# Kernel optimization log

Hardware: AMD Instinct MI355X
Metric: run time of the kernel (lower is better)

Reference implementation:

```python
import jax, jax.numpy as jnp
import numpy as np

D = 128          # hidden_dim
H = 4            # num attention heads (torch default nhead=4 in this module)
DH = D // H
NA = 4096        # author nodes
NP = 100000      # paper nodes
EAP = 500000     # author->paper edges
EPA = 500000     # paper->author edges
DFF = 2048       # TransformerEncoderLayer FFN dim (torch default)
OUT = 16
IN_A = 128
IN_P = 256
EPS = 1e-5


def layer_norm(x, g, b):
    mu = jnp.mean(x, -1, keepdims=True)
    var = jnp.mean((x - mu) ** 2, -1, keepdims=True)
    return (x - mu) / jnp.sqrt(var + EPS) * g + b


def scatter_mean(vals, idx, n):
    # torch_scatter 'mean': empty segments yield 0
    s = jax.ops.segment_sum(vals, idx, num_segments=n)
    c = jax.ops.segment_sum(jnp.ones((vals.shape[0], 1), vals.dtype), idx, num_segments=n)
    return s / jnp.maximum(c, 1.0)


def metapath_layer(x_src, x_dst, src, dst, Wv, bv, Wo, bo, g, b):
    # nn.MultiheadAttention applied per-edge with seq_len=1 (query/key/value are
    # [1, E, D]); softmax over a single key is identically 1, so the attention
    # output is exactly out_proj(v_proj(x_src[src])) -- q/k projections have no
    # effect on the output (and zero gradient).
    v = x_src[src] @ Wv.T + bv            # [E, D] gather + value projection
    attn = v @ Wo.T + bo                  # output projection
    agg = scatter_mean(attn, dst, x_dst.shape[0])
    return layer_norm(agg + x_dst, g, b)


def fusion_layer(x, Wqkv, bqkv, Wo, bo, W1, b1, W2, b2, g1, bt1, g2, bt2):
    # torch TransformerEncoderLayer defaults: post-norm, relu, batch_first=False,
    # so x: [S=NA (seq), M (batch = #metapaths), D].
    S, M, _ = x.shape
    qkv = x @ Wqkv.T + bqkv               # [S, M, 3D]
    q, k, v = jnp.split(qkv, 3, axis=-1)
    q = q.reshape(S, M, H, DH)
    k = k.reshape(S, M, H, DH)
    v = v.reshape(S, M, H, DH)
    scores = jnp.einsum('smhd,tmhd->mhst', q, k) / np.float32(np.sqrt(DH))
    a = jax.nn.softmax(scores, axis=-1)
    ctx = jnp.einsum('mhst,tmhd->smhd', a, v).reshape(S, M, D)
    x = layer_norm(x + ctx @ Wo.T + bo, g1, bt1)
    ff = jax.nn.relu(x @ W1.T + b1) @ W2.T + b2
    return layer_norm(x + ff, g2, bt2)


def setup_inputs() -> dict:
    key = jax.random.key(0)
    ks = iter(jax.random.split(key, 64))
    def nrm(shape, scale=0.02):
        return jax.random.normal(next(ks), shape, dtype=jnp.float32) * scale
    inp = {
        'x_author': jax.random.normal(next(ks), (NA, IN_A), dtype=jnp.float32),
        'x_paper': jax.random.normal(next(ks), (NP, IN_P), dtype=jnp.float32),
        'src_ap': jax.random.randint(next(ks), (EAP,), 0, NA),
        'dst_ap': jax.random.randint(next(ks), (EAP,), 0, NP),
        'src_pa': jax.random.randint(next(ks), (EPA,), 0, NP),
        'dst_pa': jax.random.randint(next(ks), (EPA,), 0, NA),
        'pa_W': nrm((D, IN_A)), 'pa_b': nrm((D,)),
        'pp_W': nrm((D, IN_P)), 'pp_b': nrm((D,)),
        'f_Wqkv': nrm((3 * D, D)), 'f_bqkv': nrm((3 * D,)),
        'f_Wo': nrm((D, D)), 'f_bo': nrm((D,)),
        'f_W1': nrm((DFF, D)), 'f_b1': nrm((DFF,)),
        'f_W2': nrm((D, DFF)), 'f_b2': nrm((D,)),
        'f_g1': jnp.ones((D,), jnp.float32), 'f_bt1': jnp.zeros((D,), jnp.float32),
        'f_g2': jnp.ones((D,), jnp.float32), 'f_bt2': jnp.zeros((D,), jnp.float32),
        'cls_W': nrm((OUT, D)), 'cls_b': nrm((OUT,)),
    }
    for i in range(3):
        inp[f'l{i}_Wv'] = nrm((D, D)); inp[f'l{i}_bv'] = nrm((D,))
        inp[f'l{i}_Wo'] = nrm((D, D)); inp[f'l{i}_bo'] = nrm((D,))
        inp[f'l{i}_g'] = jnp.ones((D,), jnp.float32); inp[f'l{i}_b'] = jnp.zeros((D,), jnp.float32)
    return inp


def reference(x_author, x_paper, src_ap, dst_ap, src_pa, dst_pa,
              pa_W, pa_b, pp_W, pp_b,
              f_Wqkv, f_bqkv, f_Wo, f_bo, f_W1, f_b1, f_W2, f_b2,
              f_g1, f_bt1, f_g2, f_bt2, cls_W, cls_b,
              l0_Wv, l0_bv, l0_Wo, l0_bo, l0_g, l0_b,
              l1_Wv, l1_bv, l1_Wo, l1_bo, l1_g, l1_b,
              l2_Wv, l2_bv, l2_Wo, l2_bo, l2_g, l2_b):
    # project node features to hidden_dim
    ha = x_author @ pa_W.T + pa_b         # [NA, D]
    hp = x_paper @ pp_W.T + pp_b          # [NP, D]
    # metapath 0: paper -> author (one MetapathLayer)
    mp0 = metapath_layer(hp, ha, src_pa, dst_pa, l0_Wv, l0_bv, l0_Wo, l0_bo, l0_g, l0_b)
    # metapath 1: author -> paper -> author (two MetapathLayers)
    t = metapath_layer(ha, hp, src_ap, dst_ap, l1_Wv, l1_bv, l1_Wo, l1_bo, l1_g, l1_b)
    mp1 = metapath_layer(t, ha, src_pa, dst_pa, l2_Wv, l2_bv, l2_Wo, l2_bo, l2_g, l2_b)
    stacked = jnp.stack([mp0, mp1], axis=1)   # [NA, 2, D]
    fused = fusion_layer(stacked, f_Wqkv, f_bqkv, f_Wo, f_bo,
                         f_W1, f_b1, f_W2, f_b2,
                         f_g1, f_bt1, f_g2, f_bt2).mean(axis=1)
    return fused @ cls_W.T + cls_b            # [NA, OUT]
```

## Files before the change

kernel.cpp:

```cpp
#include <hip/hip_runtime.h>
#include <math.h>

constexpr int NA = 4096, NP = 100000, E_AP = 500000, E_PA = 500000;
constexpr int D = 128, DFF = 2048, NOUT = 16, IN_A = 128, IN_P = 256;

typedef __attribute__((ext_vector_type(8))) short bf16x8;
typedef __attribute__((ext_vector_type(4))) float f32x4;
typedef unsigned int u32;

__device__ __forceinline__ ushort f2b(float x) {
    union { float f; unsigned u; } v; v.f = x;
    unsigned r = v.u + 0x7fff + ((v.u >> 16) & 1);
    return (ushort)(r >> 16);
}
__device__ __forceinline__ float b2f(ushort h) {
    union { unsigned u; float f; } v; v.u = (unsigned)h << 16;
    return v.f;
}
__device__ __forceinline__ u32 fbits(float x) {
    union { float f; u32 u; } v; v.f = x; return v.u;
}

__device__ __forceinline__ bf16x8 cvtfrag(float4 a, float4 b) {
    union { u32 w[4]; bf16x8 v; } r;
    asm("v_cvt_pk_bf16_f32 %0, %1, %2" : "=v"(r.w[0]) : "v"(a.x), "v"(a.y));
    asm("v_cvt_pk_bf16_f32 %0, %1, %2" : "=v"(r.w[1]) : "v"(a.z), "v"(a.w));
    asm("v_cvt_pk_bf16_f32 %0, %1, %2" : "=v"(r.w[2]) : "v"(b.x), "v"(b.y));
    asm("v_cvt_pk_bf16_f32 %0, %1, %2" : "=v"(r.w[3]) : "v"(b.z), "v"(b.w));
    return r.v;
}

#define GLL(gp, lp) __builtin_amdgcn_global_load_lds( \
    (const __attribute__((address_space(1))) u32*)(gp), \
    (__attribute__((address_space(3))) u32*)(lp), 16, 0, 0)

#define MFMA16(a, b, c) __builtin_amdgcn_mfma_f32_16x16x32_bf16((a), (b), (c), 0, 0, 0)

__global__ __launch_bounds__(256) void gemm_bf16(
    const ushort* __restrict__ Abf, const float* __restrict__ Af32, int lda,
    const ushort* __restrict__ B, int ldb,
    const float* __restrict__ bias,
    float* __restrict__ outf, ushort* __restrict__ outh, int ldc,
    int M, int N, int K, int act)
{
    __shared__ uint8_t lds[(16 + 32) * 1040];
    uint8_t* sAb = lds;
    uint8_t* sBb = lds + 16 * 1040;

    const int wave = threadIdx.x >> 6;
    const int lane = threadIdx.x & 63;
    const int l16 = lane & 15, quad = lane >> 4;
    const int row0 = blockIdx.y * 64;
    const int col0 = blockIdx.x * 128;
    const int wrg = (wave >> 1) * 2;
    const int wc0 = (wave & 1) * 64;
    const int nz = gridDim.z;
    const int ksub = K / nz;
    const int kbeg = blockIdx.z * ksub;
    const int kgrps = ksub >> 7;

    f32x4 acc[2][4] = {};

    const int sr = lane & 15, sc = lane >> 4;
    const int arow = min(row0 + lane, M - 1);
    const int ag = lane >> 4;
    uint8_t* adst = sAb + (ag * 4 + wave) * 1040 + sr * 16;

    for (int grp = 0; grp < kgrps; ++grp) {
        const int kg = kbeg + grp * 128;
        if (grp) __syncthreads();
        #pragma unroll
        for (int gg = 0; gg < 2; ++gg) {
            int g = wave * 2 + gg;
            const ushort* bp = B + (long)(col0 + g * 16 + sr) * ldb + kg + sc * 8;
            #pragma unroll
            for (int s = 0; s < 4; ++s)
                GLL(bp + s * 32, sBb + (g * 4 + s) * 1040);
        }
        if (Af32) {
            const float* ap = Af32 + (long)arow * lda + kg + wave * 32;
            #pragma unroll
            for (int q = 0; q < 4; ++q) {
                float4 f0 = *(const float4*)(ap + q * 8);
                float4 f1 = *(const float4*)(ap + q * 8 + 4);
                *(bf16x8*)(adst + q * 256) = cvtfrag(f0, f1);
            }
        } else {
            const ushort* ap = Abf + (long)arow * lda + kg + wave * 32;
            #pragma unroll
            for (int q = 0; q < 4; ++q)
                *(bf16x8*)(adst + q * 256) = *(const bf16x8*)(ap + q * 8);
        }
        __syncthreads();
        #pragma unroll
        for (int s = 0; s < 4; ++s) {
            bf16x8 af[2], bfr[4];
            #pragma unroll
            for (int i = 0; i < 2; ++i)
                af[i] = *(const bf16x8*)(sAb + ((wrg + i) * 4 + s) * 1040 + lane * 16);
            #pragma unroll
            for (int j = 0; j < 4; ++j)
                bfr[j] = *(const bf16x8*)(sBb + (((wc0 >> 4) + j) * 4 + s) * 1040 + lane * 16);
            #pragma unroll
            for (int i = 0; i < 2; ++i)
                #pragma unroll
                for (int j = 0; j < 4; ++j)
                    acc[i][j] = MFMA16(af[i], bfr[j], acc[i][j]);
        }
    }

    #pragma unroll
    for (int i = 0; i < 2; ++i) {
        #pragma unroll
        for (int r = 0; r < 4; ++r) {
            int row = row0 + wrg * 16 + i * 16 + quad * 4 + r;
            if (row >= M) continue;
            #pragma unroll
            for (int j = 0; j < 4; ++j) {
                int col = col0 + wc0 + j * 16 + l16;
                if (nz > 1) {
                    atomicAdd(&outf[(long)row * ldc + col], acc[i][j][r]);
                } else {
                    float v = acc[i][j][r] + (bias ? bias[col] : 0.f);
                    if (act) v = fmaxf(v, 0.f);
                    if (outf) outf[(long)row * ldc + col] = v;
                    if (outh) outh[(long)row * ldc + col] = f2b(v);
                }
            }
        }
    }
}

__global__ __launch_bounds__(256) void ffn_fused(
    const ushort* __restrict__ x1b,
    const ushort* __restrict__ W1b,
    const ushort* __restrict__ W2b,
    const float* __restrict__ b1,
    float* __restrict__ outf)
{
    __shared__ uint8_t lds[56 * 1040];
    uint8_t* sX  = lds;
    uint8_t* sW1 = lds + 16 * 1040;
    uint8_t* sW2 = lds + 32 * 1040;
    uint8_t* sH  = lds + 48 * 1040;

    const int wave = threadIdx.x >> 6;
    const int lane = threadIdx.x & 63;
    const int l16 = lane & 15, quad = lane >> 4;
    const int sr = lane & 15, sc = lane >> 4;
    const int row0 = blockIdx.x * 64;
    const int dbeg = blockIdx.y * 512;

    const int xg = wave >> 1;
    const int ch = wave & 1;

    {
        const ushort* xp = x1b + (long)(row0 + wave * 16 + sr) * 128 + sc * 8;
        #pragma unroll
        for (int s = 0; s < 4; ++s)
            GLL(xp + s * 32, sX + (wave * 4 + s) * 1040);
    }

    f32x4 acc2[2][4] = {};

    for (int c = 0; c < 8; ++c) {
        const int kc = dbeg + c * 64;
        {
            const ushort* w1p = W1b + (long)(kc + wave * 16 + sr) * 128 + sc * 8;
            #pragma unroll
            for (int s = 0; s < 4; ++s)
                GLL(w1p + s * 32, sW1 + (wave * 4 + s) * 1040);
            #pragma unroll
            for (int gg = 0; gg < 2; ++gg) {
                int cg = wave * 2 + gg;
                const ushort* w2p = W2b + (long)(cg * 16 + sr) * 2048 + kc + sc * 8;
                #pragma unroll
                for (int s2 = 0; s2 < 2; ++s2)
                    GLL(w2p + s2 * 32, sW2 + (cg * 2 + s2) * 1040);
            }
        }
        __syncthreads();

        f32x4 acc1[2][2] = {};
        #pragma unroll
        for (int s = 0; s < 4; ++s) {
            bf16x8 a0 = *(const bf16x8*)(sX + ((xg * 2 + 0) * 4 + s) * 1040 + lane * 16);
            bf16x8 a1 = *(const bf16x8*)(sX + ((xg * 2 + 1) * 4 + s) * 1040 + lane * 16);
            bf16x8 w0 = *(const bf16x8*)(sW1 + ((ch * 2 + 0) * 4 + s) * 1040 + lane * 16);
            bf16x8 w1 = *(const bf16x8*)(sW1 + ((ch * 2 + 1) * 4 + s) * 1040 + lane * 16);
            acc1[0][0] = MFMA16(a0, w0, acc1[0][0]);
            acc1[0][1] = MFMA16(a0, w1, acc1[0][1]);
            acc1[1][0] = MFMA16(a1, w0, acc1[1][0]);
            acc1[1][1] = MFMA16(a1, w1, acc1[1][1]);
        }
        float bb0 = b1[kc + ch * 32 + l16];
        float bb1 = b1[kc + ch * 32 + 16 + l16];
        #pragma unroll
        for (int i = 0; i < 2; ++i) {
            uint8_t* hb = sH + ((xg * 2 + i) * 2 + ch) * 1040;
            #pragma unroll
            for (int j = 0; j < 2; ++j) {
                float bb = j ? bb1 : bb0;
                int q = ((j * 16 + l16) >> 3) & 3;
                int byo = (l16 & 7) * 2;
                #pragma unroll
                for (int r = 0; r < 4; ++r) {
                    float v = fmaxf(acc1[i][j][r] + bb, 0.f);
                    *(ushort*)(hb + q * 256 + (quad * 4 + r) * 16 + byo) = f2b(v);
                }
            }
        }
        __syncthreads();

        #pragma unroll
        for (int s2 = 0; s2 < 2; ++s2) {
            bf16x8 h0 = *(const bf16x8*)(sH + ((xg * 2 + 0) * 2 + s2) * 1040 + lane * 16);
            bf16x8 h1 = *(const bf16x8*)(sH + ((xg * 2 + 1) * 2 + s2) * 1040 + lane * 16);
            #pragma unroll
            for (int j2 = 0; j2 < 4; ++j2) {
                bf16x8 wb = *(const bf16x8*)(sW2 + ((ch * 4 + j2) * 2 + s2) * 1040 + lane * 16);
                acc2[0][j2] = MFMA16(h0, wb, acc2[0][j2]);
                acc2[1][j2] = MFMA16(h1, wb, acc2[1][j2]);
            }
        }
        __syncthreads();
    }

    #pragma unroll
    for (int i = 0; i < 2; ++i)
        #pragma unroll
        for (int r = 0; r < 4; ++r) {
            int row = row0 + xg * 32 + i * 16 + quad * 4 + r;
            #pragma unroll
            for (int j2 = 0; j2 < 4; ++j2) {
                int col = ch * 64 + j2 * 16 + l16;
                atomicAdd(&outf[(long)row * 128 + col], acc2[i][j2][r]);
            }
        }
}

__global__ __launch_bounds__(256) void fuse_weights(
    const float* __restrict__ Wv0, const float* __restrict__ bv0,
    const float* __restrict__ Wo0, const float* __restrict__ bo0,
    const float* __restrict__ Wv1, const float* __restrict__ bv1,
    const float* __restrict__ Wo1, const float* __restrict__ bo1,
    const float* __restrict__ Wv2, const float* __restrict__ bv2,
    const float* __restrict__ Wo2, const float* __restrict__ bo2,
    ushort* __restrict__ Wfb, float* __restrict__ beff)
{
    int blk = blockIdx.x;
    if (blk >= 192) {
        int l = blk - 192;
        const float* bv = l == 0 ? bv0 : (l == 1 ? bv1 : bv2);
        const float* Wo = l == 0 ? Wo0 : (l == 1 ? Wo1 : Wo2);
        const float* bo = l == 0 ? bo0 : (l == 1 ? bo1 : bo2);
        if (threadIdx.x < 128) {
            int r = threadIdx.x;
            float acc = bo[r];
            #pragma unroll 8
            for (int j = 0; j < 128; ++j) acc += Wo[r * 128 + j] * bv[j];
            beff[l * 128 + r] = acc;
        }
        return;
    }
    int l = blk >> 6;
    const float* Wv = l == 0 ? Wv0 : (l == 1 ? Wv1 : Wv2);
    const float* Wo = l == 0 ? Wo0 : (l == 1 ? Wo1 : Wo2);
    int r = (blk & 63) * 2 + (threadIdx.x >> 7);
    int c = threadIdx.x & 127;
    float acc = 0.f;
    #pragma unroll 8
    for (int j = 0; j < 128; ++j)
        acc += Wo[r * 128 + j] * Wv[j * 128 + c];
    Wfb[l * 16384 + r * 128 + c] = f2b(acc);
}

__global__ void hist_kernel(const int* __restrict__ dst, int* __restrict__ cnt, int E)
{
    int e = blockIdx.x * 256 + threadIdx.x;
    if (e < E) atomicAdd(&cnt[dst[e]], 1);
}

__global__ __launch_bounds__(256) void scan_local(
    const int* __restrict__ in, int* __restrict__ out,
    int* __restrict__ bsum, int n)
{
    __shared__ int wsum[4];
    int t = threadIdx.x;
    int base = blockIdx.x * 1024 + t * 4;
    int v0 = (base + 0 < n) ? in[base + 0] : 0;
    int v1 = (base + 1 < n) ? in[base + 1] : 0;
    int v2 = (base + 2 < n) ? in[base + 2] : 0;
    int v3 = (base + 3 < n) ? in[base + 3] : 0;
    int tsum = v0 + v1 + v2 + v3;
    int lane = t & 63;
    int x = tsum;
    #pragma unroll
    for (int o = 1; o < 64; o <<= 1) {
        int y = __shfl_up(x, o, 64);
        if (lane >= o) x += y;
    }
    int wid = t >> 6;
    if (lane == 63) wsum[wid] = x;
    __syncthreads();
    int woff = 0;
    #pragma unroll
    for (int ww = 0; ww < 3; ++ww) if (ww < wid) woff += wsum[ww];
    int excl = x - tsum + woff;
    if (base + 0 < n) out[base + 0] = excl;
    if (base + 1 < n) out[base + 1] = excl + v0;
    if (base + 2 < n) out[base + 2] = excl + v0 + v1;
    if (base + 3 < n) out[base + 3] = excl + v0 + v1 + v2;
    if (bsum && t == 255) bsum[blockIdx.x] = excl + tsum;
}

__global__ void scan_add(int* __restrict__ off, const int* __restrict__ bofs,
                         int* __restrict__ cur, int n)
{
    int i = blockIdx.x * 256 + threadIdx.x;
    if (i < n) {
        int v = off[i] + bofs[i >> 10];
        off[i] = v;
        cur[i] = v;
    }
}

__global__ void fill_csr_kernel(const int* __restrict__ src, const int* __restrict__ dst,
                                int* __restrict__ cur, int* __restrict__ esrc, int E)
{
    int e = blockIdx.x * 256 + threadIdx.x;
    if (e >= E) return;
    int slot = atomicAdd(&cur[dst[e]], 1);
    esrc[slot] = src[e];
}

__global__ __launch_bounds__(256) void gather_mean(
    const ushort* __restrict__ z, const int* __restrict__ off,
    const int* __restrict__ cnt, const int* __restrict__ esrc,
    ushort* __restrict__ outh, int R)
{
    int grp = threadIdx.x >> 5;
    int tg  = threadIdx.x & 31;
    int row = blockIdx.x * 8 + grp;
    if (row >= R) return;
    int e0 = off[row], deg = cnt[row];
    int eend = e0 + deg;
    float a0 = 0.f, a1 = 0.f, a2 = 0.f, a3 = 0.f;
    int e = e0;
    for (; e + 4 <= eend; e += 4) {
        int s0 = esrc[e], s1 = esrc[e + 1], s2 = esrc[e + 2], s3 = esrc[e + 3];
        ushort4 v0 = ((const ushort4*)(z + (long)s0 * 128))[tg];
        ushort4 v1 = ((const ushort4*)(z + (long)s1 * 128))[tg];
        ushort4 v2 = ((const ushort4*)(z + (long)s2 * 128))[tg];
        ushort4 v3 = ((const ushort4*)(z + (long)s3 * 128))[tg];
        a0 += b2f(v0.x) + b2f(v1.x) + b2f(v2.x) + b2f(v3.x);
        a1 += b2f(v0.y) + b2f(v1.y) + b2f(v2.y) + b2f(v3.y);
        a2 += b2f(v0.z) + b2f(v1.z) + b2f(v2.z) + b2f(v3.z);
        a3 += b2f(v0.w) + b2f(v1.w) + b2f(v2.w) + b2f(v3.w);
    }
    for (; e < eend; ++e) {
        int s = esrc[e];
        ushort4 v = ((const ushort4*)(z + (long)s * 128))[tg];
        a0 += b2f(v.x); a1 += b2f(v.y); a2 += b2f(v.z); a3 += b2f(v.w);
    }
    float inv = 1.f / fmaxf((float)deg, 1.f);
    ushort4 h4 = {f2b(a0 * inv), f2b(a1 * inv), f2b(a2 * inv), f2b(a3 * inv)};
    ((ushort4*)(outh + (long)row * 128))[tg] = h4;
}

__global__ __launch_bounds__(256) void gather_mean_ln(
    const ushort* __restrict__ z, const int* __restrict__ off,
    const int* __restrict__ cnt, const int* __restrict__ esrc,
    const ushort* __restrict__ base, const float* __restrict__ g,
    const float* __restrict__ b, ushort* __restrict__ outh, int R)
{
    int grp = threadIdx.x >> 5;
    int tg  = threadIdx.x & 31;
    int row = blockIdx.x * 8 + grp;
    if (row >= R) return;
    int e0 = off[row], deg = cnt[row];
    int eend = e0 + deg;
    float a0 = 0.f, a1 = 0.f, a2 = 0.f, a3 = 0.f;
    int e = e0;
    for (; e + 4 <= eend; e += 4) {
        int s0 = esrc[e], s1 = esrc[e + 1], s2 = esrc[e + 2], s3 = esrc[e + 3];
        ushort4 v0 = ((const ushort4*)(z + (long)s0 * 128))[tg];
        ushort4 v1 = ((const ushort4*)(z + (long)s1 * 128))[tg];
        ushort4 v2 = ((const ushort4*)(z + (long)s2 * 128))[tg];
        ushort4 v3 = ((const ushort4*)(z + (long)s3 * 128))[tg];
        a0 += b2f(v0.x) + b2f(v1.x) + b2f(v2.x) + b2f(v3.x);
        a1 += b2f(v0.y) + b2f(v1.y) + b2f(v2.y) + b2f(v3.y);
        a2 += b2f(v0.z) + b2f(v1.z) + b2f(v2.z) + b2f(v3.z);
        a3 += b2f(v0.w) + b2f(v1.w) + b2f(v2.w) + b2f(v3.w);
    }
    for (; e < eend; ++e) {
        int s = esrc[e];
        ushort4 v = ((const ushort4*)(z + (long)s * 128))[tg];
        a0 += b2f(v.x); a1 += b2f(v.y); a2 += b2f(v.z); a3 += b2f(v.w);
    }
    float inv = 1.f / fmaxf((float)deg, 1.f);
    ushort4 bs = ((const ushort4*)(base + (long)row * 128))[tg];
    float x0 = a0 * inv + b2f(bs.x), x1 = a1 * inv + b2f(bs.y);
    float x2 = a2 * inv + b2f(bs.z), x3 = a3 * inv + b2f(bs.w);
    float s1 = x0 + x1 + x2 + x3;
    #pragma unroll
    for (int o = 1; o < 32; o <<= 1) s1 += __shfl_xor(s1, o, 64);
    float mu = s1 * (1.f / 128.f);
    float d0 = x0 - mu, d1 = x1 - mu, d2 = x2 - mu, d3 = x3 - mu;
    float s2 = d0 * d0 + d1 * d1 + d2 * d2 + d3 * d3;
    #pragma unroll
    for (int o = 1; o < 32; o <<= 1) s2 += __shfl_xor(s2, o, 64);
    float rstd = rsqrtf(s2 * (1.f / 128.f) + 1e-5f);
    float4 gv = ((const float4*)g)[tg];
    float4 bv = ((const float4*)b)[tg];
    ushort4 h4;
    h4.x = f2b(d0 * rstd * gv.x + bv.x);
    h4.y = f2b(d1 * rstd * gv.y + bv.y);
    h4.z = f2b(d2 * rstd * gv.z + bv.z);
    h4.w = f2b(d3 * rstd * gv.w + bv.w);
    ((ushort4*)(outh + (long)row * 128))[tg] = h4;
}

__global__ __launch_bounds__(128) void mean_add_ln(
    const float* __restrict__ a, const float* __restrict__ bias,
    const float* __restrict__ basef, const ushort* __restrict__ baseh,
    const float* __restrict__ g, const float* __restrict__ b,
    float* __restrict__ outf, ushort* __restrict__ outh, int out_ld, int R)
{
    int row = blockIdx.x;
    if (row >= R) return;
    int d = threadIdx.x;
    float x = a[(long)row * 128 + d];
    if (bias) x += bias[d];
    if (basef) x += basef[(long)row * 128 + d];
    if (baseh) x += b2f(baseh[(long)row * 128 + d]);

    __shared__ float red[4];
    float s = x;
    #pragma unroll
    for (int o = 32; o >= 1; o >>= 1) s += __shfl_xor(s, o, 64);
    if ((d & 63) == 0) red[d >> 6] = s;
    __syncthreads();
    float mu = (red[0] + red[1]) * (1.f / 128.f);
    float dx = x - mu;
    float s2 = dx * dx;
    #pragma unroll
    for (int o = 32; o >= 1; o >>= 1) s2 += __shfl_xor(s2, o, 64);
    if ((d & 63) == 0) red[2 + (d >> 6)] = s2;
    __syncthreads();
    float var = (red[2] + red[3]) * (1.f / 128.f);
    float v = dx * rsqrtf(var + 1e-5f) * g[d] + b[d];
    if (outf) outf[(long)row * out_ld + d] = v;
    if (outh) outh[(long)row * out_ld + d] = f2b(v);
}

struct CvtArgs { const float* in[6]; ushort* out[6]; int n4[6]; };
__global__ void cvt_multi(CvtArgs a)
{
    int j = blockIdx.y;
    int i = blockIdx.x * 256 + threadIdx.x;
    if (i >= a.n4[j]) return;
    float4 v = ((const float4*)a.in[j])[i];
    ushort4 o;
    o.x = f2b(v.x); o.y = f2b(v.y); o.z = f2b(v.z); o.w = f2b(v.w);
    ((ushort4*)a.out[j])[i] = o;
}

__global__ __launch_bounds__(256) void flash_attn(
    const ushort* __restrict__ qkvb,
    float* __restrict__ opart, float* __restrict__ lpart_g)
{
    const int qt = blockIdx.x;
    const int mh = blockIdx.y;
    const int ks = blockIdx.z;
    const int m = mh >> 2, h = mh & 3;
    const int wave = threadIdx.x >> 6;
    const int lane = threadIdx.x & 63;
    const int l16 = lane & 15, quad = lane >> 4;

    __shared__ ushort sK[2][64 * 40];
    __shared__ u32    sV[2][32 * 32];
    __shared__ u32    sP[4][16 * 32];

    const int q0 = qt * 64 + wave * 16;
    const float qs = 0.17677669529663687f * 1.4426950408889634f;
    bf16x8 qf;
    {
        bf16x8 qraw = *(const bf16x8*)(qkvb + ((long)(q0 + l16) * 2 + m) * 384 + h * 32 + quad * 8);
        #pragma unroll
        for (int j = 0; j < 8; ++j)
            qf[j] = (short)f2b(b2f((ushort)qraw[j]) * qs);
    }

    f32x4 oacc0 = {0.f, 0.f, 0.f, 0.f};
    f32x4 oacc1 = {0.f, 0.f, 0.f, 0.f};
    float lp = 0.f;

    const int skey = threadIdx.x >> 2, sseg = threadIdx.x & 3;
    const int vkp  = threadIdx.x & 31, vdc  = (threadIdx.x >> 5) * 4;
    const int kbeg = ks * (NA / 2);
    const ushort* kbase = qkvb + ((long)((kbeg + skey) * 2 + m)) * 384 + 128 + h * 32 + sseg * 8;
    const ushort* vbase = qkvb + ((long)((kbeg + vkp * 2) * 2 + m)) * 384 + 256 + h * 32 + vdc;
    const int kwo = skey * 40 + sseg * 8;
    int vwo[4];
    #pragma unroll
    for (int i = 0; i < 4; ++i)
        vwo[i] = (vdc + i) * 32 + ((((vkp >> 2) ^ ((vdc + i) & 7)) << 2) | (vkp & 3));

    bf16x8 kreg = *(const bf16x8*)(kbase);
    ushort4 v0r = *(const ushort4*)(vbase);
    ushort4 v1r = *(const ushort4*)(vbase + 768);
    *(bf16x8*)(&sK[0][kwo]) = kreg;
    sV[0][vwo[0]] = (u32)v0r.x | ((u32)v1r.x << 16);
    sV[0][vwo[1]] = (u32)v0r.y | ((u32)v1r.y << 16);
    sV[0][vwo[2]] = (u32)v0r.z | ((u32)v1r.z << 16);
    sV[0][vwo[3]] = (u32)v0r.w | ((u32)v1r.w << 16);
    __syncthreads();

    int cur = 0;
    for (int kt = 0; kt < 32; ++kt) {
        const bool more = (kt + 1) < 32;
        if (more) {
            long off = (long)(kt + 1) * 64 * 768;
            kreg = *(const bf16x8*)(kbase + off);
            v0r  = *(const ushort4*)(vbase + off);
            v1r  = *(const ushort4*)(vbase + off + 768);
        }

        #pragma unroll
        for (int t = 0; t < 4; ++t) {
            bf16x8 kf = *(const bf16x8*)(&sK[cur][(t * 16 + l16) * 40 + quad * 8]);
            f32x4 s = {0.f, 0.f, 0.f, 0.f};
            s = MFMA16(kf, qf, s);
            float p0 = exp2f(s[0]), p1 = exp2f(s[1]);
            float p2 = exp2f(s[2]), p3 = exp2f(s[3]);
            lp += (p0 + p1) + (p2 + p3);
            u32 lo = __builtin_amdgcn_perm(fbits(p1), fbits(p0), 0x07060302u);
            u32 hi = __builtin_amdgcn_perm(fbits(p3), fbits(p2), 0x07060302u);
            u32* dst = &sP[wave][l16 * 32 +
                                 ((((t * 2 + (quad >> 1)) ^ (l16 & 7)) << 2) | ((quad & 1) * 2))];
            dst[0] = lo; dst[1] = hi;
        }
        #pragma unroll
        for (int c = 0; c < 2; ++c) {
            const int gp = ((c * 4 + quad) ^ (l16 & 7)) << 2;
            bf16x8 pf  = *(const bf16x8*)(&sP[wave][l16 * 32 + gp]);
            bf16x8 vf0 = *(const bf16x8*)(&sV[cur][l16 * 32 + gp]);
            bf16x8 vf1 = *(const bf16x8*)(&sV[cur][(16 + l16) * 32 + gp]);
            oacc0 = MFMA16(pf, vf0, oacc0);
            oacc1 = MFMA16(pf, vf1, oacc1);
        }

        if (more) {
            const int nxt = cur ^ 1;
            *(bf16x8*)(&sK[nxt][kwo]) = kreg;
            sV[nxt][vwo[0]] = (u32)v0r.x | ((u32)v1r.x << 16);
            sV[nxt][vwo[1]] = (u32)v0r.y | ((u32)v1r.y << 16);
            sV[nxt][vwo[2]] = (u32)v0r.z | ((u32)v1r.z << 16);
            sV[nxt][vwo[3]] = (u32)v0r.w | ((u32)v1r.w << 16);
            __syncthreads();
            cur = nxt;
        }
    }

    lp += __shfl_xor(lp, 16, 64);
    lp += __shfl_xor(lp, 32, 64);
    if (quad == 0)
        lpart_g[(long)(mh * 2 + ks) * NA + q0 + l16] = lp;

    #pragma unroll
    for (int r = 0; r < 4; ++r) {
        int qr = q0 + quad * 4 + r;
        long ob = ((long)(mh * 2 + ks) * NA + qr) * 32;
        opart[ob + l16]      = oacc0[r];
        opart[ob + 16 + l16] = oacc1[r];
    }
}

__global__ void attn_combine(const float* __restrict__ opart,
                             const float* __restrict__ lpart,
                             ushort* __restrict__ ctxb)
{
    int idx = blockIdx.x * 256 + threadIdx.x;
    int d = idx & 31;
    int row = idx >> 5;
    int mh = row >> 12, qrow = row & 4095;
    float o = 0.f, l = 0.f;
    #pragma unroll
    for (int ks = 0; ks < 2; ++ks) {
        long rb = (long)(mh * 2 + ks) * NA + qrow;
        o += opart[rb * 32 + d];
        l += lpart[rb];
    }
    int m = mh >> 2, h = mh & 3;
    ctxb[((long)qrow * 2 + m) * 128 + h * 32 + d] = f2b(o / l);
}

__global__ void classify_kernel(const float* __restrict__ x2,
                                const float* __restrict__ Wc,
                                const float* __restrict__ bc,
                                float* __restrict__ out)
{
    int idx = blockIdx.x * 256 + threadIdx.x;
    int a2 = idx >> 4, o = idx & 15;
    const float* r0 = x2 + (long)(a2 * 2) * 128;
    const float* r1 = r0 + 128;
    const float* w = Wc + o * 128;
    float acc = bc[o];
    #pragma unroll 4
    for (int dd = 0; dd < 128; ++dd) acc += 0.5f * (r0[dd] + r1[dd]) * w[dd];
    out[idx] = acc;
}

static void bgemm(hipStream_t st, const ushort* Abf, const float* Af32, int lda,
                  const ushort* B, int ldb,
                  const float* bias, float* outf, ushort* outh, int ldc,
                  int M, int N, int K, int act = 0, int ksplit = 1)
{
    dim3 grid(N / 128, (M + 63) / 64, ksplit);
    gemm_bf16<<<grid, 256, 0, st>>>(Abf, Af32, lda, B, ldb, bias, outf, outh,
                                    ldc, M, N, K, act);
}

static void build_csr(hipStream_t st, const int* src, const int* dst, int E, int n,
                      int* cnt, int* off, int* cur, int* bsum, int* esrc)
{
    hipMemsetAsync(cnt, 0, (size_t)n * 4, st);
    hist_kernel<<<(E + 255) / 256, 256, 0, st>>>(dst, cnt, E);
    int nb = (n + 1023) / 1024;
    scan_local<<<nb, 256, 0, st>>>(cnt, off, bsum, n);
    scan_local<<<1, 256, 0, st>>>(bsum, bsum, nullptr, nb);
    scan_add<<<(n + 255) / 256, 256, 0, st>>>(off, bsum, cur, n);
    fill_csr_kernel<<<(E + 255) / 256, 256, 0, st>>>(src, dst, cur, esrc, E);
}

extern "C" void kernel_launch(void* const* d_in, const int* in_sizes, int n_in,
                              void* d_out, int out_size, void* d_ws, size_t ws_size,
                              hipStream_t stream)
{
    const float* x_author = (const float*)d_in[0];
    const float* x_paper  = (const float*)d_in[1];
    const int*   src_ap   = (const int*)d_in[2];
    const int*   dst_ap   = (const int*)d_in[3];
    const int*   src_pa   = (const int*)d_in[4];
    const int*   dst_pa   = (const int*)d_in[5];
    const float* pa_W = (const float*)d_in[6];   const float* pa_b = (const float*)d_in[7];
    const float* pp_W = (const float*)d_in[8];   const float* pp_b = (const float*)d_in[9];
    const float* f_Wqkv = (const float*)d_in[10]; const float* f_bqkv = (const float*)d_in[11];
    const float* f_Wo = (const float*)d_in[12];  const float* f_bo = (const float*)d_in[13];
    const float* f_W1 = (const float*)d_in[14];  const float* f_b1 = (const float*)d_in[15];
    const float* f_W2 = (const float*)d_in[16];  const float* f_b2 = (const float*)d_in[17];
    const float* f_g1 = (const float*)d_in[18];  const float* f_bt1 = (const float*)d_in[19];
    const float* f_g2 = (const float*)d_in[20];  const float* f_bt2 = (const float*)d_in[21];
    const float* cls_W = (const float*)d_in[22]; const float* cls_b = (const float*)d_in[23];
    const float* l0_Wv = (const float*)d_in[24]; const float* l0_bv = (const float*)d_in[25];
    const float* l0_Wo = (const float*)d_in[26]; const float* l0_bo = (const float*)d_in[27];
    const float* l0_g  = (const float*)d_in[28]; const float* l0_b  = (const float*)d_in[29];
    const float* l1_Wv = (const float*)d_in[30]; const float* l1_bv = (const float*)d_in[31];
    const float* l1_Wo = (const float*)d_in[32]; const float* l1_bo = (const float*)d_in[33];
    const float* l1_g  = (const float*)d_in[34]; const float* l1_b  = (const float*)d_in[35];
    const float* l2_Wv = (const float*)d_in[36]; const float* l2_bv = (const float*)d_in[37];
    const float* l2_Wo = (const float*)d_in[38]; const float* l2_bo = (const float*)d_in[39];
    const float* l2_g  = (const float*)d_in[40]; const float* l2_b  = (const float*)d_in[41];

    uint8_t* w = (uint8_t*)d_ws;
    ushort* TB  = (ushort*)(w + 0);
    float*  OPART = (float*)(w + 26214400);
    float*  LPART = (float*)(w + 43515904);
    ushort* HPB = (ushort*)(w + 61440000);
    ushort* ZB  = (ushort*)(w + 87040000);
    uint8_t* p2 = w + 102400000;
    ushort* QKVB = (ushort*)(p2 + 0);
    ushort* CTXB = (ushort*)(p2 + 6291456);
    float*  TMP  = (float*)(p2 + 8388608);
    float*  X1   = (float*)(p2 + 12582912);
    ushort* X1B  = (ushort*)(p2 + 16777216);
    float*  TMP2 = (float*)(p2 + 18874368);
    float*  X2   = (float*)(p2 + 23068672);
    uint8_t* tail = p2 + 27262976;
    ushort* STKB  = (ushort*)(tail + 4194304);
    ushort* HAB   = (ushort*)(tail + 6291456);
    ushort* GMA   = (ushort*)(tail + 7340032);
    ushort* WFB   = (ushort*)(tail + 8388608);
    ushort* PAWB  = (ushort*)(tail + 8486912);
    ushort* PPWB  = (ushort*)(tail + 8519680);
    ushort* WQKVB = (ushort*)(tail + 8585216);
    ushort* WOB   = (ushort*)(tail + 8683520);
    ushort* W1B   = (ushort*)(tail + 8716288);
    ushort* W2B   = (ushort*)(tail + 9240576);
    float*  BEFF  = (float*)(tail + 9764864);
    int*   CNT_A  = (int*)(tail + 9766400);
    int*   OFF_A  = (int*)(tail + 9782784);
    int*   CUR_A  = (int*)(tail + 9799168);
    int*   CNT_P  = (int*)(tail + 9815552);
    int*   OFF_P  = (int*)(tail + 10215552);
    int*   CUR_P  = (int*)(tail + 10615552);
    int*   ESRC_PA= (int*)(tail + 11015552);
    int*   ESRC_AP= (int*)(tail + 13015552);
    int*   BSUM_A = (int*)(tail + 15015552);
    int*   BSUM_P = (int*)(tail + 15016576);
    float* TMPA   = (float*)(tail + 15017984);

    CvtArgs ca;
    ca.in[0] = pa_W;   ca.out[0] = PAWB;  ca.n4[0] = D * IN_A / 4;
    ca.in[1] = pp_W;   ca.out[1] = PPWB;  ca.n4[1] = D * IN_P / 4;
    ca.in[2] = f_Wqkv; ca.out[2] = WQKVB; ca.n4[2] = 3 * D * D / 4;
    ca.in[3] = f_Wo;   ca.out[3] = WOB;   ca.n4[3] = D * D / 4;
    ca.in[4] = f_W1;   ca.out[4] = W1B;   ca.n4[4] = DFF * D / 4;
    ca.in[5] = f_W2;   ca.out[5] = W2B;   ca.n4[5] = D * DFF / 4;
    cvt_multi<<<dim3((DFF * D / 4 + 255) / 256, 6), 256, 0, stream>>>(ca);

    fuse_weights<<<195, 256, 0, stream>>>(l0_Wv, l0_bv, l0_Wo, l0_bo,
                                          l1_Wv, l1_bv, l1_Wo, l1_bo,
                                          l2_Wv, l2_bv, l2_Wo, l2_bo, WFB, BEFF);

    build_csr(stream, src_pa, dst_pa, E_PA, NA, CNT_A, OFF_A, CUR_A, BSUM_A, ESRC_PA);
    build_csr(stream, src_ap, dst_ap, E_AP, NP, CNT_P, OFF_P, CUR_P, BSUM_P, ESRC_AP);

    bgemm(stream, nullptr, x_author, IN_A, PAWB, IN_A, pa_b, nullptr, HAB, D, NA, D, IN_A);
    bgemm(stream, nullptr, x_paper,  IN_P, PPWB, IN_P, pp_b, nullptr, HPB, D, NP, D, IN_P);

    gather_mean<<<(NA + 7) / 8, 256, 0, stream>>>(HPB, OFF_A, CNT_A, ESRC_PA, GMA, NA);
    bgemm(stream, GMA, nullptr, D, WFB, D, BEFF, TMPA, nullptr, D, NA, D, D);
    mean_add_ln<<<NA, 128, 0, stream>>>(TMPA, nullptr, nullptr, HAB, l0_g, l0_b,
                                        nullptr, STKB, 256, NA);

    bgemm(stream, HAB, nullptr, D, WFB + 16384, D, BEFF + 128, nullptr, ZB, D, NA, D, D);
    gather_mean_ln<<<(NP + 7) / 8, 256, 0, stream>>>(
        ZB, OFF_P, CNT_P, ESRC_AP, HPB, l1_g, l1_b, TB, NP);

    gather_mean<<<(NA + 7) / 8, 256, 0, stream>>>(TB, OFF_A, CNT_A, ESRC_PA, GMA, NA);
    bgemm(stream, GMA, nullptr, D, WFB + 32768, D, BEFF + 256, TMPA, nullptr, D, NA, D, D);
    mean_add_ln<<<NA, 128, 0, stream>>>(TMPA, nullptr, nullptr, HAB, l2_g, l2_b,
                                        nullptr, STKB + 128, 256, NA);

    bgemm(stream, STKB, nullptr, D, WQKVB, D, f_bqkv, nullptr, QKVB, 3 * D, 2 * NA, 3 * D, D);
    flash_attn<<<dim3(NA / 64, 8, 2), 256, 0, stream>>>(QKVB, OPART, LPART);
    attn_combine<<<8 * NA * 32 / 256, 256, 0, stream>>>(OPART, LPART, CTXB);

    bgemm(stream, CTXB, nullptr, D, WOB, D, f_bo, TMP, nullptr, D, 2 * NA, D, D);
    mean_add_ln<<<2 * NA, 128, 0, stream>>>(TMP, nullptr, nullptr, STKB, f_g1, f_bt1,
                                            X1, X1B, 128, 2 * NA);

    hipMemsetAsync(TMP2, 0, (size_t)2 * NA * D * 4, stream);
    ffn_fused<<<dim3(2 * NA / 64, 4), 256, 0, stream>>>(X1B, W1B, W2B, f_b1, TMP2);
    mean_add_ln<<<2 * NA, 128, 0, stream>>>(TMP2, f_b2, X1, nullptr, f_g2, f_bt2,
                                            X2, nullptr, 128, 2 * NA);

    classify_kernel<<<(NA * NOUT) / 256, 256, 0, stream>>>(X2, cls_W, cls_b, (float*)d_out);
}
```

Before: 674.8 us.

## Split author gathers across edge chunks, merge CSR builds, stage GEMM bf16 stores via LDS

The author-side neighbour aggregation now splits each row's edge list into four chunks and accumulates fp32 sums with atomics. This gives about 125 edges per row more parallelism than one 32-lane group. The mean division and bias are moved into the following LayerNorm kernel, which now takes the degree array. The two CSR builds are merged into paired kernels indexed by blockIdx.y to cut launches, and the GEMM bf16 output path is staged through LDS for coalesced 16-byte row stores. In exchange the change adds memsets, fp32 atomics with nondeterministic summation order, and an fp32 GEMM input path.

Measured after the change: 701.7 us. +4.0%, slower.

```diff
diff --git a/kernel.cpp b/kernel.cpp
--- a/kernel.cpp
+++ b/kernel.cpp
@@ -109,6 +109,36 @@
         }
     }
 
+    if (outh && nz == 1) {
+        __syncthreads();
+        ushort* sC = (ushort*)lds;
+        #pragma unroll
+        for (int i = 0; i < 2; ++i) {
+            #pragma unroll
+            for (int r = 0; r < 4; ++r) {
+                int lrow = wrg * 16 + i * 16 + quad * 4 + r;
+                #pragma unroll
+                for (int j = 0; j < 4; ++j) {
+                    int lcol = wc0 + j * 16 + l16;
+                    float v = acc[i][j][r] + (bias ? bias[col0 + lcol] : 0.f);
+                    if (act) v = fmaxf(v, 0.f);
+                    sC[lrow * 134 + lcol] = f2b(v);
+                }
+            }
+        }
+        __syncthreads();
+        int rr = threadIdx.x >> 2, qq = threadIdx.x & 3;
+        int grow = row0 + rr;
+        if (grow < M) {
+            const ushort* src = sC + rr * 134 + qq * 32;
+            ushort* dst = outh + (long)grow * ldc + col0 + qq * 32;
+            #pragma unroll
+            for (int k = 0; k < 4; ++k)
+                *(bf16x8*)(dst + k * 8) = *(const bf16x8*)(src + k * 8);
+        }
+        return;
+    }
+
     #pragma unroll
     for (int i = 0; i < 2; ++i) {
         #pragma unroll
@@ -124,7 +154,6 @@
                     float v = acc[i][j][r] + (bias ? bias[col] : 0.f);
                     if (act) v = fmaxf(v, 0.f);
                     if (outf) outf[(long)row * ldc + col] = v;
-                    if (outh) outh[(long)row * ldc + col] = f2b(v);
                 }
             }
         }
@@ -275,16 +304,23 @@
     Wfb[l * 16384 + r * 128 + c] = f2b(acc);
 }
 
-__global__ void hist_kernel(const int* __restrict__ dst, int* __restrict__ cnt, int E)
+__global__ void hist2(const int* __restrict__ dA, int* __restrict__ cA,
+                      const int* __restrict__ dP, int* __restrict__ cP, int E)
 {
     int e = blockIdx.x * 256 + threadIdx.x;
-    if (e < E) atomicAdd(&cnt[dst[e]], 1);
-}
-
-__global__ __launch_bounds__(256) void scan_local(
-    const int* __restrict__ in, int* __restrict__ out,
-    int* __restrict__ bsum, int n)
-{
+    if (e >= E) return;
+    if (blockIdx.y == 0) atomicAdd(&cA[dA[e]], 1);
+    else                 atomicAdd(&cP[dP[e]], 1);
+}
+
+__global__ __launch_bounds__(256) void scan_local2(
+    const int* __restrict__ inA, int* __restrict__ outA, int* __restrict__ bsumA, int nA,
+    const int* __restrict__ inP, int* __restrict__ outP, int* __restrict__ bsumP, int nP)
+{
+    const int* in  = blockIdx.y ? inP  : inA;
+    int* out       = blockIdx.y ? outP : outA;
+    int* bsum      = blockIdx.y ? bsumP : bsumA;
+    int n          = blockIdx.y ? nP : nA;
     __shared__ int wsum[4];
     int t = threadIdx.x;
     int base = blockIdx.x * 1024 + t * 4;
@@ -314,9 +350,15 @@
     if (bsum && t == 255) bsum[blockIdx.x] = excl + tsum;
 }
 
-__global__ void scan_add(int* __restrict__ off, const int* __restrict__ bofs,
-                         int* __restrict__ cur, int n)
-{
+__global__ void scan_add2(int* __restrict__ offA, const int* __restrict__ bA,
+                          int* __restrict__ curA, int nA,
+                          int* __restrict__ offP, const int* __restrict__ bP,
+                          int* __restrict__ curP, int nP)
+{
+    int* off       = blockIdx.y ? offP : offA;
+    const int* bofs= blockIdx.y ? bP   : bA;
+    int* cur       = blockIdx.y ? curP : curA;
+    int n          = blockIdx.y ? nP : nA;
     int i = blockIdx.x * 256 + threadIdx.x;
     if (i < n) {
         int v = off[i] + bofs[i >> 10];
@@ -325,19 +367,59 @@
     }
 }
 
-__global__ void fill_csr_kernel(const int* __restrict__ src, const int* __restrict__ dst,
-                                int* __restrict__ cur, int* __restrict__ esrc, int E)
+__global__ void fill2(const int* __restrict__ sA, const int* __restrict__ dA,
+                      int* __restrict__ cuA, int* __restrict__ eA,
+                      const int* __restrict__ sP, const int* __restrict__ dP,
+                      int* __restrict__ cuP, int* __restrict__ eP, int E)
 {
     int e = blockIdx.x * 256 + threadIdx.x;
     if (e >= E) return;
-    int slot = atomicAdd(&cur[dst[e]], 1);
-    esrc[slot] = src[e];
-}
-
-__global__ __launch_bounds__(256) void gather_mean(
+    if (blockIdx.y == 0) { int slot = atomicAdd(&cuA[dA[e]], 1); eA[slot] = sA[e]; }
+    else                 { int slot = atomicAdd(&cuP[dP[e]], 1); eP[slot] = sP[e]; }
+}
+
+__global__ __launch_bounds__(256) void gather_sum(
     const ushort* __restrict__ z, const int* __restrict__ off,
     const int* __restrict__ cnt, const int* __restrict__ esrc,
-    ushort* __restrict__ outh, int R)
+    float* __restrict__ outf, int R)
+{
+    int grp = threadIdx.x >> 5;
+    int tg  = threadIdx.x & 31;
+    int gid = blockIdx.x * 8 + grp;
+    int row = gid >> 2, chunk = gid & 3;
+    if (row >= R) return;
+    int e0 = off[row], deg = cnt[row];
+    int c0 = e0 + (int)(((long)deg * chunk) >> 2);
+    int c1 = e0 + (int)(((long)deg * (chunk + 1)) >> 2);
+    if (c0 >= c1) return;
+    float a0 = 0.f, a1 = 0.f, a2 = 0.f, a3 = 0.f;
+    int e = c0;
+    for (; e + 4 <= c1; e += 4) {
+        int s0 = esrc[e], s1 = esrc[e + 1], s2 = esrc[e + 2], s3 = esrc[e + 3];
+        ushort4 v0 = ((const ushort4*)(z + (long)s0 * 128))[tg];
+        ushort4 v1 = ((const ushort4*)(z + (long)s1 * 128))[tg];
+        ushort4 v2 = ((const ushort4*)(z + (long)s2 * 128))[tg];
+        ushort4 v3 = ((const ushort4*)(z + (long)s3 * 128))[tg];
+        a0 += b2f(v0.x) + b2f(v1.x) + b2f(v2.x) + b2f(v3.x);
+        a1 += b2f(v0.y) + b2f(v1.y) + b2f(v2.y) + b2f(v3.y);
+        a2 += b2f(v0.z) + b2f(v1.z) + b2f(v2.z) + b2f(v3.z);
+        a3 += b2f(v0.w) + b2f(v1.w) + b2f(v2.w) + b2f(v3.w);
+    }
+    for (; e < c1; ++e) {
+        int s = esrc[e];
+        ushort4 v = ((const ushort4*)(z + (long)s * 128))[tg];
+        a0 += b2f(v.x); a1 += b2f(v.y); a2 += b2f(v.z); a3 += b2f(v.w);
+    }
+    float* op = outf + (long)row * 128 + tg * 4;
+    atomicAdd(op + 0, a0); atomicAdd(op + 1, a1);
+    atomicAdd(op + 2, a2); atomicAdd(op + 3, a3);
+}
+
+__global__ __launch_bounds__(256) void gather_mean_ln(
+    const ushort* __restrict__ z, const int* __restrict__ off,
+    const int* __restrict__ cnt, const int* __restrict__ esrc,
+    const ushort* __restrict__ base, const float* __restrict__ g,
+    const float* __restrict__ b, ushort* __restrict__ outh, int R)
 {
     int grp = threadIdx.x >> 5;
     int tg  = threadIdx.x & 31;
@@ -364,41 +446,6 @@
         a0 += b2f(v.x); a1 += b2f(v.y); a2 += b2f(v.z); a3 += b2f(v.w);
     }
     float inv = 1.f / fmaxf((float)deg, 1.f);
-    ushort4 h4 = {f2b(a0 * inv), f2b(a1 * inv), f2b(a2 * inv), f2b(a3 * inv)};
-    ((ushort4*)(outh + (long)row * 128))[tg] = h4;
-}
-
-__global__ __launch_bounds__(256) void gather_mean_ln(
-    const ushort* __restrict__ z, const int* __restrict__ off,
-    const int* __restrict__ cnt, const int* __restrict__ esrc,
-    const ushort* __restrict__ base, const float* __restrict__ g,
-    const float* __restrict__ b, ushort* __restrict__ outh, int R)
-{
-    int grp = threadIdx.x >> 5;
-    int tg  = threadIdx.x & 31;
-    int row = blockIdx.x * 8 + grp;
-    if (row >= R) return;
-    int e0 = off[row], deg = cnt[row];
-    int eend = e0 + deg;
-    float a0 = 0.f, a1 = 0.f, a2 = 0.f, a3 = 0.f;
-    int e = e0;
-    for (; e + 4 <= eend; e += 4) {
-        int s0 = esrc[e], s1 = esrc[e + 1], s2 = esrc[e + 2], s3 = esrc[e + 3];
-        ushort4 v0 = ((const ushort4*)(z + (long)s0 * 128))[tg];
-        ushort4 v1 = ((const ushort4*)(z + (long)s1 * 128))[tg];
-        ushort4 v2 = ((const ushort4*)(z + (long)s2 * 128))[tg];
-        ushort4 v3 = ((const ushort4*)(z + (long)s3 * 128))[tg];
-        a0 += b2f(v0.x) + b2f(v1.x) + b2f(v2.x) + b2f(v3.x);
-        a1 += b2f(v0.y) + b2f(v1.y) + b2f(v2.y) + b2f(v3.y);
-        a2 += b2f(v0.z) + b2f(v1.z) + b2f(v2.z) + b2f(v3.z);
-        a3 += b2f(v0.w) + b2f(v1.w) + b2f(v2.w) + b2f(v3.w);
-    }
-    for (; e < eend; ++e) {
-        int s = esrc[e];
-        ushort4 v = ((const ushort4*)(z + (long)s * 128))[tg];
-        a0 += b2f(v.x); a1 += b2f(v.y); a2 += b2f(v.z); a3 += b2f(v.w);
-    }
-    float inv = 1.f / fmaxf((float)deg, 1.f);
     ushort4 bs = ((const ushort4*)(base + (long)row * 128))[tg];
     float x0 = a0 * inv + b2f(bs.x), x1 = a1 * inv + b2f(bs.y);
     float x2 = a2 * inv + b2f(bs.z), x3 = a3 * inv + b2f(bs.w);
@@ -425,12 +472,14 @@
     const float* __restrict__ a, const float* __restrict__ bias,
     const float* __restrict__ basef, const ushort* __restrict__ baseh,
     const float* __restrict__ g, const float* __restrict__ b,
-    float* __restrict__ outf, ushort* __restrict__ outh, int out_ld, int R)
+    float* __restrict__ outf, ushort* __restrict__ outh, int out_ld, int R,
+    const int* __restrict__ degp)
 {
     int row = blockIdx.x;
     if (row >= R) return;
     int d = threadIdx.x;
     float x = a[(long)row * 128 + d];
+    if (degp) x *= 1.f / fmaxf((float)degp[row], 1.f);
     if (bias) x += bias[d];
     if (basef) x += basef[(long)row * 128 + d];
     if (baseh) x += b2f(baseh[(long)row * 128 + d]);
@@ -620,18 +669,6 @@
     dim3 grid(N / 128, (M + 63) / 64, ksplit);
     gemm_bf16<<<grid, 256, 0, st>>>(Abf, Af32, lda, B, ldb, bias, outf, outh,
                                     ldc, M, N, K, act);
-}
-
-static void build_csr(hipStream_t st, const int* src, const int* dst, int E, int n,
-                      int* cnt, int* off, int* cur, int* bsum, int* esrc)
-{
-    hipMemsetAsync(cnt, 0, (size_t)n * 4, st);
-    hist_kernel<<<(E + 255) / 256, 256, 0, st>>>(dst, cnt, E);
-    int nb = (n + 1023) / 1024;
-    scan_local<<<nb, 256, 0, st>>>(cnt, off, bsum, n);
-    scan_local<<<1, 256, 0, st>>>(bsum, bsum, nullptr, nb);
-    scan_add<<<(n + 255) / 256, 256, 0, st>>>(off, bsum, cur, n);
-    fill_csr_kernel<<<(E + 255) / 256, 256, 0, st>>>(src, dst, cur, esrc, E);
 }
 
 extern "C" void kernel_launch(void* const* d_in, const int* in_sizes, int n_in,
@@ -673,6 +710,7 @@
     ushort* QKVB = (ushort*)(p2 + 0);
     ushort* CTXB = (ushort*)(p2 + 6291456);
     float*  TMP  = (float*)(p2 + 8388608);
+    float*  GMA32= (float*)(p2 + 8388608);
     float*  X1   = (float*)(p2 + 12582912);
     ushort* X1B  = (ushort*)(p2 + 16777216);
     float*  TMP2 = (float*)(p2 + 18874368);
@@ -680,7 +718,6 @@
     uint8_t* tail = p2 + 27262976;
     ushort* STKB  = (ushort*)(tail + 4194304);
     ushort* HAB   = (ushort*)(tail + 6291456);
-    ushort* GMA   = (ushort*)(tail + 7340032);
     ushort* WFB   = (ushort*)(tail + 8388608);
     ushort* PAWB  = (ushort*)(tail + 8486912);
     ushort* PPWB  = (ushort*)(tail + 8519680);
@@ -714,25 +751,37 @@
                                           l1_Wv, l1_bv, l1_Wo, l1_bo,
                                           l2_Wv, l2_bv, l2_Wo, l2_bo, WFB, BEFF);
 
-    build_csr(stream, src_pa, dst_pa, E_PA, NA, CNT_A, OFF_A, CUR_A, BSUM_A, ESRC_PA);
-    build_csr(stream, src_ap, dst_ap, E_AP, NP, CNT_P, OFF_P, CUR_P, BSUM_P, ESRC_AP);
+    hipMemsetAsync(CNT_A, 0, (size_t)NA * 4, stream);
+    hipMemsetAsync(CNT_P, 0, (size_t)NP * 4, stream);
+    const int nbA = (NA + 1023) / 1024, nbP = (NP + 1023) / 1024;
+    hist2<<<dim3((E_PA + 255) / 256, 2), 256, 0, stream>>>(dst_pa, CNT_A, dst_ap, CNT_P, E_PA);
+    scan_local2<<<dim3(nbP, 2), 256, 0, stream>>>(CNT_A, OFF_A, BSUM_A, NA,
+                                                  CNT_P, OFF_P, BSUM_P, NP);
+    scan_local2<<<dim3(1, 2), 256, 0, stream>>>(BSUM_A, BSUM_A, nullptr, nbA,
+                                                BSUM_P, BSUM_P, nullptr, nbP);
+    scan_add2<<<dim3((NP + 255) / 256, 2), 256, 0, stream>>>(OFF_A, BSUM_A, CUR_A, NA,
+                                                             OFF_P, BSUM_P, CUR_P, NP);
+    fill2<<<dim3((E_PA + 255) / 256, 2), 256, 0, stream>>>(
+        src_pa, dst_pa, CUR_A, ESRC_PA, src_ap, dst_ap, CUR_P, ESRC_AP, E_PA);
 
     bgemm(stream, nullptr, x_author, IN_A, PAWB, IN_A, pa_b, nullptr, HAB, D, NA, D, IN_A);
     bgemm(stream, nullptr, x_paper,  IN_P, PPWB, IN_P, pp_b, nullptr, HPB, D, NP, D, IN_P);
 
-    gather_mean<<<(NA + 7) / 8, 256, 0, stream>>>(HPB, OFF_A, CNT_A, ESRC_PA, GMA, NA);
-    bgemm(stream, GMA, nullptr, D, WFB, D, BEFF, TMPA, nullptr, D, NA, D, D);
-    mean_add_ln<<<NA, 128, 0, stream>>>(TMPA, nullptr, nullptr, HAB, l0_g, l0_b,
-                                        nullptr, STKB, 256, NA);
+    hipMemsetAsync(GMA32, 0, (size_t)NA * D * 4, stream);
+    gather_sum<<<(NA * 4 + 7) / 8, 256, 0, stream>>>(HPB, OFF_A, CNT_A, ESRC_PA, GMA32, NA);
+    bgemm(stream, nullptr, GMA32, D, WFB, D, nullptr, TMPA, nullptr, D, NA, D, D);
+    mean_add_ln<<<NA, 128, 0, stream>>>(TMPA, BEFF, nullptr, HAB, l0_g, l0_b,
+                                        nullptr, STKB, 256, NA, CNT_A);
 
     bgemm(stream, HAB, nullptr, D, WFB + 16384, D, BEFF + 128, nullptr, ZB, D, NA, D, D);
     gather_mean_ln<<<(NP + 7) / 8, 256, 0, stream>>>(
         ZB, OFF_P, CNT_P, ESRC_AP, HPB, l1_g, l1_b, TB, NP);
 
-    gather_mean<<<(NA + 7) / 8, 256, 0, stream>>>(TB, OFF_A, CNT_A, ESRC_PA, GMA, NA);
-    bgemm(stream, GMA, nullptr, D, WFB + 32768, D, BEFF + 256, TMPA, nullptr, D, NA, D, D);
-    mean_add_ln<<<NA, 128, 0, stream>>>(TMPA, nullptr, nullptr, HAB, l2_g, l2_b,
-                                        nullptr, STKB + 128, 256, NA);
+    hipMemsetAsync(GMA32, 0, (size_t)NA * D * 4, stream);
+    gather_sum<<<(NA * 4 + 7) / 8, 256, 0, stream>>>(TB, OFF_A, CNT_A, ESRC_PA, GMA32, NA);
+    bgemm(stream, nullptr, GMA32, D, WFB + 32768, D, nullptr, TMPA, nullptr, D, NA, D, D);
+    mean_add_ln<<<NA, 128, 0, stream>>>(TMPA, BEFF + 256, nullptr, HAB, l2_g, l2_b,
+                                        nullptr, STKB + 128, 256, NA, CNT_A);
 
     bgemm(stream, STKB, nullptr, D, WQKVB, D, f_bqkv, nullptr, QKVB, 3 * D, 2 * NA, 3 * D, D);
     flash_attn<<<dim3(NA / 64, 8, 2), 256, 0, stream>>>(QKVB, OPART, LPART);
@@ -740,12 +789,12 @@
 
     bgemm(stream, CTXB, nullptr, D, WOB, D, f_bo, TMP, nullptr, D, 2 * NA, D, D);
     mean_add_ln<<<2 * NA, 128, 0, stream>>>(TMP, nullptr, nullptr, STKB, f_g1, f_bt1,
-                                            X1, X1B, 128, 2 * NA);
+                                            X1, X1B, 128, 2 * NA, nullptr);
 
     hipMemsetAsync(TMP2, 0, (size_t)2 * NA * D * 4, stream);
     ffn_fused<<<dim3(2 * NA / 64, 4), 256, 0, stream>>>(X1B, W1B, W2B, f_b1, TMP2);
     mean_add_ln<<<2 * NA, 128, 0, stream>>>(TMP2, f_b2, X1, nullptr, f_g2, f_bt2,
-                                            X2, nullptr, 128, 2 * NA);
+                                            X2, nullptr, 128, 2 * NA, nullptr);
 
     classify_kernel<<<(NA * NOUT) / 256, 256, 0, stream>>>(X2, cls_W, cls_b, (float*)d_out);
 }
```
